# Kernel optimization log

Hardware: AMD Instinct MI355X
Metric: run time of the kernel (lower is better)

Reference implementation:

```python
import jax, jax.numpy as jnp
import numpy as np

EPS = 1e-5
_INV_STD = 1.0 / np.sqrt(1.0 + EPS)  # eval-mode BN with running_mean=0, running_var=1


def conv1x1(x, w):
    # x: (B,C,H,W), w: (O,C) -> (B,O,H,W)
    return jnp.einsum('bchw,oc->bohw', x, w)


def bn_relu(x, gamma, beta):
    y = x * (_INV_STD * gamma)[None, :, None, None] + beta[None, :, None, None]
    return jax.nn.relu(y)


def setup_inputs() -> dict:
    key = jax.random.key(0)
    ks = jax.random.split(key, 8)
    B, C, H, W, Kc, Kp = 8, 512, 128, 128, 256, 19
    s = 0.02
    return {
        'x': jax.random.normal(ks[0], (B, C, H, W), jnp.float32),
        'proxy_feats': jax.random.normal(ks[1], (B, C, Kp, 1), jnp.float32),
        'wq1': jax.random.normal(ks[2], (Kc, C), jnp.float32) * s,
        'gq1': jnp.ones((Kc,), jnp.float32), 'bq1': jnp.zeros((Kc,), jnp.float32),
        'wq2': jax.random.normal(ks[3], (Kc, Kc), jnp.float32) * s,
        'gq2': jnp.ones((Kc,), jnp.float32), 'bq2': jnp.zeros((Kc,), jnp.float32),
        'wk1': jax.random.normal(ks[4], (Kc, C), jnp.float32) * s,
        'gk1': jnp.ones((Kc,), jnp.float32), 'bk1': jnp.zeros((Kc,), jnp.float32),
        'wk2': jax.random.normal(ks[5], (Kc, Kc), jnp.float32) * s,
        'gk2': jnp.ones((Kc,), jnp.float32), 'bk2': jnp.zeros((Kc,), jnp.float32),
        'wv': jax.random.normal(ks[6], (Kc, C), jnp.float32) * s,
        'gv': jnp.ones((Kc,), jnp.float32), 'bv': jnp.zeros((Kc,), jnp.float32),
        'wo': jax.random.normal(ks[7], (C, Kc), jnp.float32) * s,
        'go': jnp.ones((C,), jnp.float32), 'bo': jnp.zeros((C,), jnp.float32),
    }


def reference(x, proxy_feats, wq1, gq1, bq1, wq2, gq2, bq2,
              wk1, gk1, bk1, wk2, gk2, bk2, wv, gv, bv, wo, go, bo):
    B, C, H, W = x.shape
    Kc = wq1.shape[0]
    # projections: 1x1 conv -> BN(eval) -> ReLU chains
    q = bn_relu(conv1x1(bn_relu(conv1x1(x, wq1), gq1, bq1), wq2), gq2, bq2)          # (B,Kc,H,W)
    k = bn_relu(conv1x1(bn_relu(conv1x1(proxy_feats, wk1), gk1, bk1), wk2), gk2, bk2)[..., 0]  # (B,Kc,Kp)
    v = bn_relu(conv1x1(proxy_feats, wv), gv, bv)[..., 0]                             # (B,Kc,Kp)
    qf = q.reshape(B, Kc, H * W).transpose(0, 2, 1)                                   # (B,HW,Kc)
    sim = jnp.einsum('bnc,bck->bnk', qf, k) * (Kc ** -0.5)                            # (B,HW,Kp)
    att = jax.nn.softmax(sim, axis=-1)
    ctx = jnp.einsum('bnk,bck->bnc', att, v)                                          # (B,HW,Kc)
    ctx = ctx.transpose(0, 2, 1).reshape(B, Kc, H, W)
    return bn_relu(conv1x1(ctx, wo), go, bo)                                          # (B,C,H,W)
```

## Files before the change

### kernel.cpp

```cpp
#include <hip/hip_runtime.h>

#define INV_STD 0.9999950000374997f

typedef unsigned short u16;
typedef __bf16 bf16x8 __attribute__((ext_vector_type(8)));
typedef __bf16 bf16x4 __attribute__((ext_vector_type(4)));
typedef float f32x4 __attribute__((ext_vector_type(4)));

__device__ __forceinline__ u16 f2bf(float f) {
    unsigned int u = __float_as_uint(f);
    u += 0x7fffu + ((u >> 16) & 1u);
    return (u16)(u >> 16);
}

__device__ __forceinline__ void gl_lds16(const void* g, void* l) {
    __builtin_amdgcn_global_load_lds(
        (const __attribute__((address_space(1))) unsigned int*)(unsigned long long)g,
        (__attribute__((address_space(3))) unsigned int*)(unsigned int)(unsigned long long)l,
        16, 0, 0);
}

__device__ __forceinline__ f32x4 mfma16(bf16x8 a, bf16x8 b, f32x4 c) {
    return __builtin_amdgcn_mfma_f32_16x16x32_bf16(a, b, c, 0, 0, 0);
}

__device__ __forceinline__ unsigned lds_off(const void* p) {
    return (unsigned)(unsigned long long)p;
}

__device__ __forceinline__ bf16x4 tr_read(unsigned addr) {
    bf16x4 r;
    asm volatile("ds_read_b64_tr_b16 %0, %1" : "=v"(r) : "v"(addr));
    return r;
}

__device__ __forceinline__ bf16x8 ldg8(const u16* p) {
    return *(const bf16x8*)p;
}

__global__ void wprep(const float* __restrict__ wq1, const float* __restrict__ gq1,
                      const float* __restrict__ wq2, const float* __restrict__ gq2,
                      const float* __restrict__ wo,  const float* __restrict__ go,
                      u16* __restrict__ WQ1B, u16* __restrict__ WQ2B, u16* __restrict__ WOB) {
    int blk = blockIdx.x;
    int t = threadIdx.x;
    if (blk < 512) {
        long i = (long)blk * 256 + t;
        int o = (int)(i >> 9);
        int q = (int)(i & 511);
        int r = q & 31;
        int src = (q & ~31) + ((r >> 3) & 3) * 4 + (r & 3) + ((r >> 2) & 1) * 16;
        WQ1B[i] = f2bf(wq1[(long)o * 512 + src] * (INV_STD * gq1[o]));
    } else if (blk < 768) {
        long i = (long)(blk - 512) * 256 + t;
        int o = (int)(i >> 8);
        WQ2B[i] = f2bf(wq2[i] * (INV_STD * gq2[o]));
    } else {
        long i = (long)(blk - 768) * 256 + t;
        int o = (int)(i >> 8);
        WOB[i] = f2bf(wo[i] * (INV_STD * go[o]));
    }
}

__global__ __launch_bounds__(256) void kv_kernel(
    const float* __restrict__ proxy,
    const float* __restrict__ wk1, const float* __restrict__ gk1, const float* __restrict__ bk1,
    const float* __restrict__ wk2, const float* __restrict__ gk2, const float* __restrict__ bk2,
    const float* __restrict__ wv,  const float* __restrict__ gv,  const float* __restrict__ bv,
    u16* __restrict__ KB,
    u16* __restrict__ VB)
{
    int b = blockIdx.x >> 5, p = blockIdx.x & 31;
    int t = threadIdx.x;
    if (p >= 19) {
        KB[((long)b * 32 + p) * 256 + t] = 0;
        VB[((long)b * 256 + t) * 32 + p] = 0;
        return;
    }
    __shared__ float px[512];
    __shared__ float k1[256];
    for (int i = t; i < 512; i += 256) px[i] = proxy[((long)b * 512 + i) * 19 + p];
    __syncthreads();
    float aK = 0.f, aV = 0.f;
    const float4* wk1r = (const float4*)(wk1 + (long)t * 512);
    const float4* wvr  = (const float4*)(wv  + (long)t * 512);
    const float4* pxv  = (const float4*)px;
    #pragma unroll 4
    for (int c = 0; c < 128; ++c) {
        float4 pv = pxv[c];
        float4 k4 = wk1r[c];
        float4 v4 = wvr[c];
        aK += k4.x * pv.x + k4.y * pv.y + k4.z * pv.z + k4.w * pv.w;
        aV += v4.x * pv.x + v4.y * pv.y + v4.z * pv.z + v4.w * pv.w;
    }
    float k1v = fmaxf(aK * (INV_STD * gk1[t]) + bk1[t], 0.f);
    float vv  = fmaxf(aV * (INV_STD * gv[t])  + bv[t],  0.f);
    k1[t] = k1v;
    VB[((long)b * 256 + t) * 32 + p] = f2bf(vv);
    __syncthreads();
    float a2 = 0.f;
    const float4* wk2r = (const float4*)(wk2 + (long)t * 256);
    const float4* k1v4 = (const float4*)k1;
    #pragma unroll 4
    for (int c = 0; c < 64; ++c) {
        float4 w4 = wk2r[c];
        float4 kk = k1v4[c];
        a2 += w4.x * kk.x + w4.y * kk.y + w4.z * kk.z + w4.w * kk.w;
    }
    KB[((long)b * 32 + p) * 256 + t] = f2bf(fmaxf(a2 * (INV_STD * gk2[t]) + bk2[t], 0.f));
}

__global__ __launch_bounds__(256, 2) void fused_all(
    const float* __restrict__ X,
    const u16* __restrict__ W1,
    const float* __restrict__ b1,
    const u16* __restrict__ W2,
    const float* __restrict__ b2,
    const u16* __restrict__ KB,
    const u16* __restrict__ VB,
    const u16* __restrict__ Wo,
    const float* __restrict__ obias,
    float* __restrict__ out)
{
    __shared__ __align__(16) u16 xs[64 * 64];
    __shared__ __align__(16) u16 lB[2][256 * 32];
    __shared__ __align__(16) u16 q12s[64 * 264];
    __shared__ __align__(16) u16 atts[64 * 40];
    int t = threadIdx.x, lane = t & 63, w = t >> 6;
    int l16 = lane & 15, hi = lane >> 4;
    long m0 = (long)blockIdx.x * 64;
    int b = (int)(m0 >> 14);
    int pixg = (int)(m0 & 16383);
    const float* xb = X + (long)b * 512 * 16384 + pixg;
    int ca = t >> 4;
    int aa = t & 15;
    int rW = lane >> 2;
    int cW = (lane & 3) << 3;
    unsigned trb = lds_off(&xs[hi * 64 + l16]);

    {
        f32x4 acc[4][4] = {};
        float4 xr0, xr1, xr2, xr3;
        {
            const float* p0 = xb + (long)ca * 16384 + aa * 4;
            xr0 = *(const float4*)(p0);
            xr1 = *(const float4*)(p0 + 16L * 16384);
            xr2 = *(const float4*)(p0 + 32L * 16384);
            xr3 = *(const float4*)(p0 + 48L * 16384);
        }
        #define STW(XR, P) { \
            int c = (P) * 16 + ca; \
            ushort4 u; u.x = f2bf(XR.x); u.y = f2bf(XR.y); u.z = f2bf(XR.z); u.w = f2bf(XR.w); \
            *(ushort4*)&xs[((aa >> 2) * 16 + (c >> 2)) * 64 + (c & 3) * 16 + (aa & 3) * 4] = u; }
        for (int kt = 0; kt < 8; ++kt) {
            int k0 = kt << 6;
            if (kt > 0) __syncthreads();
            STW(xr0, 0) STW(xr1, 1) STW(xr2, 2) STW(xr3, 3)
            __syncthreads();
            bf16x8 bb0[4], bb1[4];
            #pragma unroll
            for (int j = 0; j < 4; ++j) {
                const u16* wr = W1 + (long)(w * 64 + j * 16 + l16) * 512 + k0 + hi * 8;
                bb0[j] = ldg8(wr);
                bb1[j] = ldg8(wr + 32);
            }
            if (kt < 7) {
                const float* p0 = xb + (long)(k0 + 64 + ca) * 16384 + aa * 4;
                xr0 = *(const float4*)(p0);
                xr1 = *(const float4*)(p0 + 16L * 16384);
                xr2 = *(const float4*)(p0 + 32L * 16384);
                xr3 = *(const float4*)(p0 + 48L * 16384);
            }
            bf16x4 lo0[4], hh0[4], lo1[4], hh1[4];
            #pragma unroll
            for (int i = 0; i < 4; ++i) {
                unsigned a0 = trb + i * 2048;
                lo0[i] = tr_read(a0);
                hh0[i] = tr_read(a0 + 512);
            }
            #pragma unroll
            for (int i = 0; i < 4; ++i) {
                unsigned a0 = trb + i * 2048 + 1024;
                lo1[i] = tr_read(a0);
                hh1[i] = tr_read(a0 + 512);
            }
            asm volatile("s_waitcnt lgkmcnt(8)" ::: "memory");
            __builtin_amdgcn_sched_barrier(0);
            #pragma unroll
            for (int i = 0; i < 4; ++i) {
                bf16x8 a = __builtin_shufflevector(lo0[i], hh0[i], 0, 1, 2, 3, 4, 5, 6, 7);
                #pragma unroll
                for (int j = 0; j < 4; ++j)
                    acc[i][j] = mfma16(a, bb0[j], acc[i][j]);
            }
            asm volatile("s_waitcnt lgkmcnt(0)" ::: "memory");
            __builtin_amdgcn_sched_barrier(0);
            #pragma unroll
            for (int i = 0; i < 4; ++i) {
                bf16x8 a = __builtin_shufflevector(lo1[i], hh1[i], 0, 1, 2, 3, 4, 5, 6, 7);
                #pragma unroll
                for (int j = 0; j < 4; ++j)
                    acc[i][j] = mfma16(a, bb1[j], acc[i][j]);
            }
        }
        #undef STW
        #pragma unroll
        for (int j = 0; j < 4; ++j) {
            int q = w * 4 + j;
            gl_lds16(W2 + (long)(q * 16 + rW) * 256 + cW, &lB[0][q * 512]);
        }
        float bj[4];
        #pragma unroll
        for (int j = 0; j < 4; ++j) bj[j] = b1[w * 64 + j * 16 + l16];
        #pragma unroll
        for (int i = 0; i < 4; ++i)
            #pragma unroll
            for (int r = 0; r < 4; ++r) {
                int pix = i * 16 + hi * 4 + r;
                #pragma unroll
                for (int j = 0; j < 4; ++j) {
                    float v = acc[i][j][r] + bj[j];
                    q12s[pix * 264 + w * 64 + j * 16 + l16] = f2bf(fmaxf(v, 0.f));
                }
            }
    }
    __syncthreads();
    {
        f32x4 acc[4][4] = {};
        #pragma unroll
        for (int c = 0; c < 8; ++c) {
            int cur = c & 1;
            if (c < 7) {
                int k1 = (c + 1) << 5;
                #pragma unroll
                for (int j = 0; j < 4; ++j) {
                    int q = w * 4 + j;
                    gl_lds16(W2 + (long)(q * 16 + rW) * 256 + k1 + cW, &lB[cur ^ 1][q * 512]);
                }
            }
            bf16x8 a[4], bb[4];
            #pragma unroll
            for (int i = 0; i < 4; ++i)
                a[i] = *(const bf16x8*)&q12s[(i * 16 + l16) * 264 + (c << 5) + hi * 8];
            #pragma unroll
            for (int j = 0; j < 4; ++j)
                bb[j] = *(const bf16x8*)&lB[cur][(w * 64 + j * 16 + l16) * 32 + hi * 8];
            #pragma unroll
            for (int i = 0; i < 4; ++i)
                #pragma unroll
                for (int j = 0; j < 4; ++j)
                    acc[i][j] = mfma16(a[i], bb[j], acc[i][j]);
            __syncthreads();
        }
        float bj[4];
        #pragma unroll
        for (int j = 0; j < 4; ++j) bj[j] = b2[w * 64 + j * 16 + l16];
        #pragma unroll
        for (int i = 0; i < 4; ++i)
            #pragma unroll
            for (int r = 0; r < 4; ++r) {
                int pix = i * 16 + hi * 4 + r;
                #pragma unroll
                for (int j = 0; j < 4; ++j) {
                    float v = acc[i][j][r] + bj[j];
                    q12s[pix * 264 + w * 64 + j * 16 + l16] = f2bf(fmaxf(v, 0.f));
                }
            }
    }
    __syncthreads();
    {
        f32x4 s0 = {}, s1 = {};
        #pragma unroll
        for (int ks = 0; ks < 8; ++ks) {
            bf16x8 a = *(const bf16x8*)&q12s[(w * 16 + l16) * 264 + ks * 32 + hi * 8];
            bf16x8 b0 = ldg8(KB + ((long)b * 32 + l16) * 256 + ks * 32 + hi * 8);
            bf16x8 b1v = ldg8(KB + ((long)b * 32 + 16 + l16) * 256 + ks * 32 + hi * 8);
            s0 = mfma16(a, b0, s0);
            s1 = mfma16(a, b1v, s1);
        }
        const float scale = 0.0625f;
        #pragma unroll
        for (int r = 0; r < 4; ++r) {
            float v0 = s0[r] * scale;
            float v1 = s1[r] * scale;
            float mx = fmaxf(v0, v1);
            mx = fmaxf(mx, __shfl_xor(mx, 1));
            mx = fmaxf(mx, __shfl_xor(mx, 2));
            mx = fmaxf(mx, __shfl_xor(mx, 4));
            mx = fmaxf(mx, __shfl_xor(mx, 8));
            float e0 = __expf(v0 - mx);
            float e1 = (l16 < 3) ? __expf(v1 - mx) : 0.f;
            float s = e0 + e1;
            s += __shfl_xor(s, 1);
            s += __shfl_xor(s, 2);
            s += __shfl_xor(s, 4);
            s += __shfl_xor(s, 8);
            float inv = 1.f / s;
            int pix = w * 16 + hi * 4 + r;
            atts[pix * 40 + l16] = f2bf(e0 * inv);
            atts[pix * 40 + 16 + l16] = (l16 < 3) ? f2bf(e1 * inv) : (u16)0;
        }
    }
    __syncthreads();
    {
        f32x4 c4[4][4] = {};
        bf16x8 av[4], bv[4];
        #pragma unroll
        for (int mf = 0; mf < 4; ++mf)
            av[mf] = *(const bf16x8*)&atts[(mf * 16 + l16) * 40 + hi * 8];
        #pragma unroll
        for (int nf = 0; nf < 4; ++nf)
            bv[nf] = ldg8(VB + ((long)b * 256 + w * 64 + nf * 16 + l16) * 32 + hi * 8);
        #pragma unroll
        for (int mf = 0; mf < 4; ++mf)
            #pragma unroll
            for (int nf = 0; nf < 4; ++nf)
                c4[mf][nf] = mfma16(av[mf], bv[nf], c4[mf][nf]);
        #pragma unroll
        for (int mf = 0; mf < 4; ++mf)
            #pragma unroll
            for (int r = 0; r < 4; ++r) {
                int pix = mf * 16 + hi * 4 + r;
                #pragma unroll
                for (int nf = 0; nf < 4; ++nf)
                    q12s[pix * 264 + w * 64 + nf * 16 + l16] = f2bf(c4[mf][nf][r]);
            }
        #pragma unroll
        for (int j = 0; j < 4; ++j) {
            int q = w * 4 + j;
            gl_lds16(Wo + (long)(q * 16 + rW) * 256 + cW, &lB[0][q * 512]);
        }
    }
    __syncthreads();
    {
        f32x4 acc2[4][4] = {};
        #pragma unroll
        for (int cc = 0; cc < 16; ++cc) {
            int cur = cc & 1;
            if (cc < 15) {
                int nc = cc + 1;
                #pragma unroll
                for (int j = 0; j < 4; ++j) {
                    int q = w * 4 + j;
                    gl_lds16(Wo + (long)((nc >> 3) * 256 + q * 16 + rW) * 256 + ((nc & 7) << 5) + cW,
                             &lB[cur ^ 1][q * 512]);
                }
            }
            int k0 = (cc & 7) << 5;
            bf16x8 a[4], bb[4];
            #pragma unroll
            for (int m = 0; m < 4; ++m)
                a[m] = *(const bf16x8*)&q12s[(m * 16 + l16) * 264 + k0 + hi * 8];
            #pragma unroll
            for (int n = 0; n < 4; ++n)
                bb[n] = *(const bf16x8*)&lB[cur][(w * 64 + n * 16 + l16) * 32 + hi * 8];
            #pragma unroll
            for (int m = 0; m < 4; ++m)
                #pragma unroll
                for (int n = 0; n < 4; ++n)
                    acc2[m][n] = mfma16(a[m], bb[n], acc2[m][n]);
            if ((cc & 7) == 7) {
                int half = cc >> 3;
                #pragma unroll
                for (int n = 0; n < 4; ++n) {
                    int ch = half * 256 + w * 64 + n * 16 + l16;
                    float bc = obias[ch];
                    float* orow = out + ((long)b * 512 + ch) * 16384 + pixg;
                    #pragma unroll
                    for (int m = 0; m < 4; ++m) {
                        float4 v;
                        v.x = fmaxf(acc2[m][n][0] + bc, 0.f);
                        v.y = fmaxf(acc2[m][n][1] + bc, 0.f);
                        v.z = fmaxf(acc2[m][n][2] + bc, 0.f);
                        v.w = fmaxf(acc2[m][n][3] + bc, 0.f);
                        *(float4*)&orow[m * 16 + hi * 4] = v;
                    }
                }
                #pragma unroll
                for (int m = 0; m < 4; ++m)
                    #pragma unroll
                    for (int n = 0; n < 4; ++n)
                        acc2[m][n] = (f32x4){0.f, 0.f, 0.f, 0.f};
            }
            __syncthreads();
        }
    }
}

extern "C" void kernel_launch(void* const* d_in, const int* in_sizes, int n_in,
                              void* d_out, int out_size, void* d_ws, size_t ws_size,
                              hipStream_t stream) {
    const float* x    = (const float*)d_in[0];
    const float* prox = (const float*)d_in[1];
    const float* wq1  = (const float*)d_in[2];
    const float* gq1  = (const float*)d_in[3];
    const float* bq1  = (const float*)d_in[4];
    const float* wq2  = (const float*)d_in[5];
    const float* gq2  = (const float*)d_in[6];
    const float* bq2  = (const float*)d_in[7];
    const float* wk1  = (const float*)d_in[8];
    const float* gk1  = (const float*)d_in[9];
    const float* bk1  = (const float*)d_in[10];
    const float* wk2  = (const float*)d_in[11];
    const float* gk2  = (const float*)d_in[12];
    const float* bk2  = (const float*)d_in[13];
    const float* wv   = (const float*)d_in[14];
    const float* gv   = (const float*)d_in[15];
    const float* bv   = (const float*)d_in[16];
    const float* wo   = (const float*)d_in[17];
    const float* go   = (const float*)d_in[18];
    const float* bo   = (const float*)d_in[19];
    float* out = (float*)d_out;

    char* ws = (char*)d_ws;
    u16* KB   = (u16*)(ws);
    u16* VB   = KB + 65536;
    u16* WQ1B = VB + 65536;
    u16* WQ2B = WQ1B + 131072;
    u16* WOB  = WQ2B + 65536;

    wprep<<<1280, 256, 0, stream>>>(wq1, gq1, wq2, gq2, wo, go, WQ1B, WQ2B, WOB);
    kv_kernel<<<256, 256, 0, stream>>>(prox, wk1, gk1, bk1, wk2, gk2, bk2, wv, gv, bv, KB, VB);
    fused_all<<<2048, 256, 0, stream>>>(x, WQ1B, bq1, WQ2B, bq2, KB, VB, WOB, bo, out);
}
```

Before: 245.1 us.

## Load W2/Wo fragments directly to registers, drop LDS staging and syncs

Removes the double-buffered LDS staging of the W2 and Wo weight tiles, which were filled with global_load_lds. Each wave now loads its own B-fragments straight from global memory into registers, with a one-step register prefetch. This drops the per-chunk __syncthreads in both GEMM loops and frees 32 KB of LDS, so launch bounds rise to 3 blocks per CU for more occupancy. In exchange, register pressure increases under the tighter bound, and the weights are read from L2 in a less coalesced pattern (16-byte pieces spread across rows).

```diff
diff --git a/kernel.cpp b/kernel.cpp
--- a/kernel.cpp
+++ b/kernel.cpp
@@ -11,13 +11,6 @@
     unsigned int u = __float_as_uint(f);
     u += 0x7fffu + ((u >> 16) & 1u);
     return (u16)(u >> 16);
-}
-
-__device__ __forceinline__ void gl_lds16(const void* g, void* l) {
-    __builtin_amdgcn_global_load_lds(
-        (const __attribute__((address_space(1))) unsigned int*)(unsigned long long)g,
-        (__attribute__((address_space(3))) unsigned int*)(unsigned int)(unsigned long long)l,
-        16, 0, 0);
 }
 
 __device__ __forceinline__ f32x4 mfma16(bf16x8 a, bf16x8 b, f32x4 c) {
@@ -110,7 +103,7 @@
     KB[((long)b * 32 + p) * 256 + t] = f2bf(fmaxf(a2 * (INV_STD * gk2[t]) + bk2[t], 0.f));
 }
 
-__global__ __launch_bounds__(256, 2) void fused_all(
+__global__ __launch_bounds__(256, 3) void fused_all(
     const float* __restrict__ X,
     const u16* __restrict__ W1,
     const float* __restrict__ b1,
@@ -123,7 +116,6 @@
     float* __restrict__ out)
 {
     __shared__ __align__(16) u16 xs[64 * 64];
-    __shared__ __align__(16) u16 lB[2][256 * 32];
     __shared__ __align__(16) u16 q12s[64 * 264];
     __shared__ __align__(16) u16 atts[64 * 40];
     int t = threadIdx.x, lane = t & 63, w = t >> 6;
@@ -134,8 +126,6 @@
     const float* xb = X + (long)b * 512 * 16384 + pixg;
     int ca = t >> 4;
     int aa = t & 15;
-    int rW = lane >> 2;
-    int cW = (lane & 3) << 3;
     unsigned trb = lds_off(&xs[hi * 64 + l16]);
 
     {
@@ -204,11 +194,6 @@
             }
         }
         #undef STW
-        #pragma unroll
-        for (int j = 0; j < 4; ++j) {
-            int q = w * 4 + j;
-            gl_lds16(W2 + (long)(q * 16 + rW) * 256 + cW, &lB[0][q * 512]);
-        }
         float bj[4];
         #pragma unroll
         for (int j = 0; j < 4; ++j) bj[j] = b1[w * 64 + j * 16 + l16];
@@ -227,31 +212,33 @@
     __syncthreads();
     {
         f32x4 acc[4][4] = {};
+        bf16x8 wc[4], wn[4];
+        #pragma unroll
+        for (int j = 0; j < 4; ++j)
+            wc[j] = ldg8(W2 + (long)(w * 64 + j * 16 + l16) * 256 + hi * 8);
         #pragma unroll
         for (int c = 0; c < 8; ++c) {
-            int cur = c & 1;
             if (c < 7) {
                 int k1 = (c + 1) << 5;
                 #pragma unroll
-                for (int j = 0; j < 4; ++j) {
-                    int q = w * 4 + j;
-                    gl_lds16(W2 + (long)(q * 16 + rW) * 256 + k1 + cW, &lB[cur ^ 1][q * 512]);
-                }
-            }
-            bf16x8 a[4], bb[4];
+                for (int j = 0; j < 4; ++j)
+                    wn[j] = ldg8(W2 + (long)(w * 64 + j * 16 + l16) * 256 + k1 + hi * 8);
+            }
+            bf16x8 a[4];
             #pragma unroll
             for (int i = 0; i < 4; ++i)
                 a[i] = *(const bf16x8*)&q12s[(i * 16 + l16) * 264 + (c << 5) + hi * 8];
             #pragma unroll
-            for (int j = 0; j < 4; ++j)
-                bb[j] = *(const bf16x8*)&lB[cur][(w * 64 + j * 16 + l16) * 32 + hi * 8];
-            #pragma unroll
             for (int i = 0; i < 4; ++i)
                 #pragma unroll
                 for (int j = 0; j < 4; ++j)
-                    acc[i][j] = mfma16(a[i], bb[j], acc[i][j]);
-            __syncthreads();
-        }
+                    acc[i][j] = mfma16(a[i], wc[j], acc[i][j]);
+            if (c < 7) {
+                #pragma unroll
+                for (int j = 0; j < 4; ++j) wc[j] = wn[j];
+            }
+        }
+        __syncthreads();
         float bj[4];
         #pragma unroll
         for (int j = 0; j < 4; ++j) bj[j] = b2[w * 64 + j * 16 + l16];
@@ -325,40 +312,33 @@
                 for (int nf = 0; nf < 4; ++nf)
                     q12s[pix * 264 + w * 64 + nf * 16 + l16] = f2bf(c4[mf][nf][r]);
             }
-        #pragma unroll
-        for (int j = 0; j < 4; ++j) {
-            int q = w * 4 + j;
-            gl_lds16(Wo + (long)(q * 16 + rW) * 256 + cW, &lB[0][q * 512]);
-        }
     }
     __syncthreads();
     {
         f32x4 acc2[4][4] = {};
+        bf16x8 wc[4], wn[4];
+        #pragma unroll
+        for (int n = 0; n < 4; ++n)
+            wc[n] = ldg8(Wo + (long)(w * 64 + n * 16 + l16) * 256 + hi * 8);
         #pragma unroll
         for (int cc = 0; cc < 16; ++cc) {
-            int cur = cc & 1;
             if (cc < 15) {
                 int nc = cc + 1;
                 #pragma unroll
-                for (int j = 0; j < 4; ++j) {
-                    int q = w * 4 + j;
-                    gl_lds16(Wo + (long)((nc >> 3) * 256 + q * 16 + rW) * 256 + ((nc & 7) << 5) + cW,
-                             &lB[cur ^ 1][q * 512]);
-                }
+                for (int n = 0; n < 4; ++n)
+                    wn[n] = ldg8(Wo + (long)((nc >> 3) * 256 + w * 64 + n * 16 + l16) * 256
+                                 + ((nc & 7) << 5) + hi * 8);
             }
             int k0 = (cc & 7) << 5;
-            bf16x8 a[4], bb[4];
+            bf16x8 a[4];
             #pragma unroll
             for (int m = 0; m < 4; ++m)
                 a[m] = *(const bf16x8*)&q12s[(m * 16 + l16) * 264 + k0 + hi * 8];
             #pragma unroll
-            for (int n = 0; n < 4; ++n)
-                bb[n] = *(const bf16x8*)&lB[cur][(w * 64 + n * 16 + l16) * 32 + hi * 8];
-            #pragma unroll
             for (int m = 0; m < 4; ++m)
                 #pragma unroll
                 for (int n = 0; n < 4; ++n)
-                    acc2[m][n] = mfma16(a[m], bb[n], acc2[m][n]);
+                    acc2[m][n] = mfma16(a[m], wc[n], acc2[m][n]);
             if ((cc & 7) == 7) {
                 int half = cc >> 3;
                 #pragma unroll
@@ -382,7 +362,10 @@
                     for (int n = 0; n < 4; ++n)
                         acc2[m][n] = (f32x4){0.f, 0.f, 0.f, 0.f};
             }
-            __syncthreads();
+            if (cc < 15) {
+                #pragma unroll
+                for (int n = 0; n < 4; ++n) wc[n] = wn[n];
+            }
         }
     }
 }
```

New measurement: 291.7 us. 1.19x slower.

## Fold output projection into V by precomputing Wo·V per batch

Applied to the files above, without the earlier changes.

Uses associativity to precompute Wo·V (512x19 per batch, with the BN scale folded in) in a new small kernel, so the fused kernel does attention·(WoV) directly. This removes the 256-wide context intermediate, its LDS staging, and the 16-step Wo GEMM loop with double-buffered loads and barriers from every tile. In exchange it adds a serial small kernel that uses only 16 blocks, and the final projection now consumes bf16-rounded WoV, which changes the rounding path.

```diff
diff --git a/kernel.cpp b/kernel.cpp
--- a/kernel.cpp
+++ b/kernel.cpp
@@ -40,8 +40,7 @@
 
 __global__ void wprep(const float* __restrict__ wq1, const float* __restrict__ gq1,
                       const float* __restrict__ wq2, const float* __restrict__ gq2,
-                      const float* __restrict__ wo,  const float* __restrict__ go,
-                      u16* __restrict__ WQ1B, u16* __restrict__ WQ2B, u16* __restrict__ WOB) {
+                      u16* __restrict__ WQ1B, u16* __restrict__ WQ2B) {
     int blk = blockIdx.x;
     int t = threadIdx.x;
     if (blk < 512) {
@@ -51,14 +50,10 @@
         int r = q & 31;
         int src = (q & ~31) + ((r >> 3) & 3) * 4 + (r & 3) + ((r >> 2) & 1) * 16;
         WQ1B[i] = f2bf(wq1[(long)o * 512 + src] * (INV_STD * gq1[o]));
-    } else if (blk < 768) {
+    } else {
         long i = (long)(blk - 512) * 256 + t;
         int o = (int)(i >> 8);
         WQ2B[i] = f2bf(wq2[i] * (INV_STD * gq2[o]));
-    } else {
-        long i = (long)(blk - 768) * 256 + t;
-        int o = (int)(i >> 8);
-        WOB[i] = f2bf(wo[i] * (INV_STD * go[o]));
     }
 }
 
@@ -68,13 +63,13 @@
     const float* __restrict__ wk2, const float* __restrict__ gk2, const float* __restrict__ bk2,
     const float* __restrict__ wv,  const float* __restrict__ gv,  const float* __restrict__ bv,
     u16* __restrict__ KB,
-    u16* __restrict__ VB)
+    float* __restrict__ VF)
 {
     int b = blockIdx.x >> 5, p = blockIdx.x & 31;
     int t = threadIdx.x;
     if (p >= 19) {
         KB[((long)b * 32 + p) * 256 + t] = 0;
-        VB[((long)b * 256 + t) * 32 + p] = 0;
+        VF[((long)b * 256 + t) * 32 + p] = 0.f;
         return;
     }
     __shared__ float px[512];
@@ -96,7 +91,7 @@
     float k1v = fmaxf(aK * (INV_STD * gk1[t]) + bk1[t], 0.f);
     float vv  = fmaxf(aV * (INV_STD * gv[t])  + bv[t],  0.f);
     k1[t] = k1v;
-    VB[((long)b * 256 + t) * 32 + p] = f2bf(vv);
+    VF[((long)b * 256 + t) * 32 + p] = vv;
     __syncthreads();
     float a2 = 0.f;
     const float4* wk2r = (const float4*)(wk2 + (long)t * 256);
@@ -110,6 +105,37 @@
     KB[((long)b * 32 + p) * 256 + t] = f2bf(fmaxf(a2 * (INV_STD * gk2[t]) + bk2[t], 0.f));
 }
 
+__global__ __launch_bounds__(256) void wov_kernel(
+    const float* __restrict__ wo,
+    const float* __restrict__ go,
+    const float* __restrict__ VF,
+    u16* __restrict__ WoVB)
+{
+    int b = blockIdx.x >> 1, half = blockIdx.x & 1;
+    __shared__ float vs[256 * 20];
+    int t = threadIdx.x;
+    #pragma unroll
+    for (int p = 0; p < 19; ++p)
+        vs[t * 20 + p] = VF[((long)b * 256 + t) * 32 + p];
+    __syncthreads();
+    int ch = half * 256 + t;
+    float g = INV_STD * go[ch];
+    const float* wr = wo + (long)ch * 256;
+    float acc[19];
+    #pragma unroll
+    for (int p = 0; p < 19; ++p) acc[p] = 0.f;
+    for (int c = 0; c < 256; ++c) {
+        float wv = wr[c];
+        #pragma unroll
+        for (int p = 0; p < 19; ++p) acc[p] += wv * vs[c * 20 + p];
+    }
+    u16* dst = WoVB + ((long)b * 512 + ch) * 32;
+    #pragma unroll
+    for (int p = 0; p < 19; ++p) dst[p] = f2bf(g * acc[p]);
+    #pragma unroll
+    for (int p = 19; p < 32; ++p) dst[p] = 0;
+}
+
 __global__ __launch_bounds__(256, 2) void fused_all(
     const float* __restrict__ X,
     const u16* __restrict__ W1,
@@ -117,8 +143,7 @@
     const u16* __restrict__ W2,
     const float* __restrict__ b2,
     const u16* __restrict__ KB,
-    const u16* __restrict__ VB,
-    const u16* __restrict__ Wo,
+    const u16* __restrict__ WoVB,
     const float* __restrict__ obias,
     float* __restrict__ out)
 {
@@ -303,86 +328,28 @@
     }
     __syncthreads();
     {
-        f32x4 c4[4][4] = {};
-        bf16x8 av[4], bv[4];
+        bf16x8 av[4], bv[8];
         #pragma unroll
         for (int mf = 0; mf < 4; ++mf)
             av[mf] = *(const bf16x8*)&atts[(mf * 16 + l16) * 40 + hi * 8];
         #pragma unroll
-        for (int nf = 0; nf < 4; ++nf)
-            bv[nf] = ldg8(VB + ((long)b * 256 + w * 64 + nf * 16 + l16) * 32 + hi * 8);
-        #pragma unroll
-        for (int mf = 0; mf < 4; ++mf)
-            #pragma unroll
-            for (int nf = 0; nf < 4; ++nf)
-                c4[mf][nf] = mfma16(av[mf], bv[nf], c4[mf][nf]);
-        #pragma unroll
-        for (int mf = 0; mf < 4; ++mf)
-            #pragma unroll
-            for (int r = 0; r < 4; ++r) {
-                int pix = mf * 16 + hi * 4 + r;
-                #pragma unroll
-                for (int nf = 0; nf < 4; ++nf)
-                    q12s[pix * 264 + w * 64 + nf * 16 + l16] = f2bf(c4[mf][nf][r]);
-            }
-        #pragma unroll
-        for (int j = 0; j < 4; ++j) {
-            int q = w * 4 + j;
-            gl_lds16(Wo + (long)(q * 16 + rW) * 256 + cW, &lB[0][q * 512]);
-        }
-    }
-    __syncthreads();
-    {
-        f32x4 acc2[4][4] = {};
-        #pragma unroll
-        for (int cc = 0; cc < 16; ++cc) {
-            int cur = cc & 1;
-            if (cc < 15) {
-                int nc = cc + 1;
-                #pragma unroll
-                for (int j = 0; j < 4; ++j) {
-                    int q = w * 4 + j;
-                    gl_lds16(Wo + (long)((nc >> 3) * 256 + q * 16 + rW) * 256 + ((nc & 7) << 5) + cW,
-                             &lB[cur ^ 1][q * 512]);
-                }
-            }
-            int k0 = (cc & 7) << 5;
-            bf16x8 a[4], bb[4];
-            #pragma unroll
-            for (int m = 0; m < 4; ++m)
-                a[m] = *(const bf16x8*)&q12s[(m * 16 + l16) * 264 + k0 + hi * 8];
-            #pragma unroll
-            for (int n = 0; n < 4; ++n)
-                bb[n] = *(const bf16x8*)&lB[cur][(w * 64 + n * 16 + l16) * 32 + hi * 8];
-            #pragma unroll
-            for (int m = 0; m < 4; ++m)
-                #pragma unroll
-                for (int n = 0; n < 4; ++n)
-                    acc2[m][n] = mfma16(a[m], bb[n], acc2[m][n]);
-            if ((cc & 7) == 7) {
-                int half = cc >> 3;
-                #pragma unroll
-                for (int n = 0; n < 4; ++n) {
-                    int ch = half * 256 + w * 64 + n * 16 + l16;
-                    float bc = obias[ch];
-                    float* orow = out + ((long)b * 512 + ch) * 16384 + pixg;
-                    #pragma unroll
-                    for (int m = 0; m < 4; ++m) {
-                        float4 v;
-                        v.x = fmaxf(acc2[m][n][0] + bc, 0.f);
-                        v.y = fmaxf(acc2[m][n][1] + bc, 0.f);
-                        v.z = fmaxf(acc2[m][n][2] + bc, 0.f);
-                        v.w = fmaxf(acc2[m][n][3] + bc, 0.f);
-                        *(float4*)&orow[m * 16 + hi * 4] = v;
-                    }
-                }
-                #pragma unroll
-                for (int m = 0; m < 4; ++m)
-                    #pragma unroll
-                    for (int n = 0; n < 4; ++n)
-                        acc2[m][n] = (f32x4){0.f, 0.f, 0.f, 0.f};
-            }
-            __syncthreads();
+        for (int nf = 0; nf < 8; ++nf)
+            bv[nf] = ldg8(WoVB + ((long)b * 512 + w * 128 + nf * 16 + l16) * 32 + hi * 8);
+        #pragma unroll
+        for (int nf = 0; nf < 8; ++nf) {
+            int ch = w * 128 + nf * 16 + l16;
+            float bc = obias[ch];
+            float* orow = out + ((long)b * 512 + ch) * 16384 + pixg;
+            #pragma unroll
+            for (int mf = 0; mf < 4; ++mf) {
+                f32x4 acc = mfma16(av[mf], bv[nf], (f32x4){0.f, 0.f, 0.f, 0.f});
+                float4 v;
+                v.x = fmaxf(acc[0] + bc, 0.f);
+                v.y = fmaxf(acc[1] + bc, 0.f);
+                v.z = fmaxf(acc[2] + bc, 0.f);
+                v.w = fmaxf(acc[3] + bc, 0.f);
+                *(float4*)&orow[mf * 16 + hi * 4] = v;
+            }
         }
     }
 }
@@ -413,13 +380,14 @@
     float* out = (float*)d_out;
 
     char* ws = (char*)d_ws;
-    u16* KB   = (u16*)(ws);
-    u16* VB   = KB + 65536;
-    u16* WQ1B = VB + 65536;
-    u16* WQ2B = WQ1B + 131072;
-    u16* WOB  = WQ2B + 65536;
-
-    wprep<<<1280, 256, 0, stream>>>(wq1, gq1, wq2, gq2, wo, go, WQ1B, WQ2B, WOB);
-    kv_kernel<<<256, 256, 0, stream>>>(prox, wk1, gk1, bk1, wk2, gk2, bk2, wv, gv, bv, KB, VB);
-    fused_all<<<2048, 256, 0, stream>>>(x, WQ1B, bq1, WQ2B, bq2, KB, VB, WOB, bo, out);
-}
+    u16*   KB   = (u16*)(ws);
+    float* VF   = (float*)(ws + 131072);
+    u16*   WoVB = (u16*)(ws + 393216);
+    u16*   WQ1B = (u16*)(ws + 655360);
+    u16*   WQ2B = (u16*)(ws + 917504);
+
+    wprep<<<768, 256, 0, stream>>>(wq1, gq1, wq2, gq2, WQ1B, WQ2B);
+    kv_kernel<<<256, 256, 0, stream>>>(prox, wk1, gk1, bk1, wk2, gk2, bk2, wv, gv, bv, KB, VF);
+    wov_kernel<<<16, 256, 0, stream>>>(wo, go, VF, WoVB);
+    fused_all<<<2048, 256, 0, stream>>>(x, WQ1B, bq1, WQ2B, bq2, KB, WoVB, bo, out);
+}
```

Result: faster. 235.6 us (-3.9%).
